# Performance work log

Measured on AMD Instinct MI355X. Metric: run time of the kernel, lower is better.

Reference implementation:

```python
import jax, jax.numpy as jnp
import numpy as np

B, C, H, W, K = 8, 128, 128, 128, 7


def _ln2d(x, gamma=None, beta=None, eps=1e-5):
    # LayerNorm2d: normalize over the channel dim at each (b, h, w) position
    mu = x.mean(axis=1, keepdims=True)
    var = x.var(axis=1, keepdims=True)
    y = (x - mu) * jax.lax.rsqrt(var + eps)
    if gamma is not None:
        y = y * gamma[None, :, None, None] + beta[None, :, None, None]
    return y


def _conv1x1(x, w, b):
    # w: [C_out, C_in] (1x1 conv collapsed)
    return jnp.einsum('oi,bihw->bohw', w, x) + b[None, :, None, None]


def _sym_conv(x, w):
    # channel-symmetric 7x7 conv, padding 'same' (SymmetricConv2d, symmetry_type='channel')
    ws = 0.5 * (w + jnp.swapaxes(w, 0, 1))
    return jax.lax.conv_general_dilated(
        x, ws, window_strides=(1, 1), padding='SAME',
        dimension_numbers=('NCHW', 'OIHW', 'NCHW'))


def setup_inputs() -> dict:
    key = jax.random.key(0)
    ks = jax.random.split(key, 8)
    f32 = jnp.float32
    return {
        'ff_input': jax.random.normal(ks[0], (B, C, H, W), f32),
        'h_exc': jax.random.normal(ks[1], (B, C, H, W), f32),
        'h_inh': jax.random.normal(ks[2], (B, C, H, W), f32),
        # 1x1 gate convs over concat([h_exc, h_inh, ff]) -> C channels
        'W_gain': jax.random.normal(ks[3], (C, 3 * C), f32) * 0.02,
        'b_gain': jnp.zeros((C,), f32),
        'W_mix': jax.random.normal(ks[4], (C, 3 * C), f32) * 0.02,
        'b_mix': jnp.zeros((C,), f32),
        # symmetric 7x7 horizontal connections
        'W_inh': jax.random.normal(ks[5], (C, C, K, K), f32) * 0.01,
        'W_exc': jax.random.normal(ks[6], (C, C, K, K), f32) * 0.01,
        # static circuit parameters (use_dynamic_parameters=False)
        'alpha': jnp.zeros((C,), f32),
        'mu': jnp.zeros((C,), f32),
        'kappa': jnp.ones((C,), f32) * 0.1,
        'omega': jnp.ones((C,), f32) * 0.1,
        # affine LayerNorm2d for circuit outputs c1/c2
        'c1_gamma': jnp.ones((C,), f32), 'c1_beta': jnp.zeros((C,), f32),
        'c2_gamma': jnp.ones((C,), f32), 'c2_beta': jnp.zeros((C,), f32),
    }


def reference(ff_input, h_exc, h_inh, W_gain, b_gain, W_mix, b_mix,
              W_inh, W_exc, alpha, mu, kappa, omega,
              c1_gamma, c1_beta, c2_gamma, c2_beta):
    # --- stage 1: gain gate (pre-norm on concat, 1x1 conv, sigmoid) ---
    g1_in = _ln2d(jnp.concatenate([h_exc, h_inh, ff_input], axis=1))  # [B,3C,H,W]
    g1 = jax.nn.sigmoid(_conv1x1(g1_in, W_gain, b_gain))              # [B,C,H,W]

    # --- stage 2: horizontal inhibition from gain-controlled excitatory state ---
    c1 = _ln2d(_sym_conv(h_exc * g1, W_inh), c1_gamma, c1_beta)

    # --- stage 3: input integration: divisive (alpha) + subtractive (mu) inhibition ---
    a = jax.nn.sigmoid(alpha)[None, :, None, None]  # force_alpha_divisive
    m = mu[None, :, None, None]
    inhibited = jax.nn.relu(ff_input - jax.nn.relu((a * h_inh + m) * c1))

    # --- stage 4: mix gate ---
    g2_in = _ln2d(jnp.concatenate([inhibited, h_exc, h_inh], axis=1))
    g2 = jax.nn.sigmoid(_conv1x1(g2_in, W_mix, b_mix))

    # --- stage 5: excitatory horizontal connections ---
    c2 = _ln2d(_sym_conv(inhibited, W_exc), c2_gamma, c2_beta)

    # --- stage 6: output integration (multiplicative excitation) ---
    k = kappa[None, :, None, None]
    o = jax.nn.relu(omega)[None, :, None, None]  # force_omega_nonnegative
    h_tilde = jax.nn.relu(k * (inhibited + c2) + o * (inhibited * c2))

    # --- gated state update of the excitatory population ---
    h_exc_new = (1.0 - g2) * h_exc + g2 * h_tilde
    return h_exc_new
```

## Files before the change

kernel.cpp:

```cpp
#include <hip/hip_runtime.h>
#include <cstddef>
#include <cstdint>

namespace {
constexpr int B_ = 8, C_ = 128, H_ = 128, W_ = 128;
constexpr int HW_ = H_ * W_;
constexpr size_t CHW_ = (size_t)C_ * HW_;
constexpr int NPIX_ = B_ * HW_;
}

typedef __attribute__((ext_vector_type(8))) short bf16x8;
typedef __attribute__((ext_vector_type(4))) float f32x4;
typedef __attribute__((ext_vector_type(2))) float f32x2;
typedef __attribute__((ext_vector_type(8))) unsigned short u16x8;
typedef __attribute__((ext_vector_type(4))) unsigned short u16x4;

__device__ inline unsigned short f2bf(float f) {
  unsigned int u = __float_as_uint(f);
  unsigned int r = u + 0x7FFFu + ((u >> 16) & 1u);
  return (unsigned short)(r >> 16);
}
__device__ inline float bf2f(unsigned short u) {
  return __uint_as_float((unsigned int)u << 16);
}

__device__ inline void async_copy16(void* lds_dst, const void* gsrc) {
  __builtin_amdgcn_global_load_lds(
      (const __attribute__((address_space(1))) unsigned int*)gsrc,
      (__attribute__((address_space(3))) unsigned int*)lds_dst, 16, 0, 0);
}

__global__ __launch_bounds__(256) void prep_w_bf16_k(
    const float* __restrict__ Wa, const float* __restrict__ Wb,
    unsigned short* __restrict__ Ta, unsigned short* __restrict__ Tb) {
  int idx = blockIdx.x * 256 + threadIdx.x;
  int j = idx & 7;
  int o = (idx >> 3) & 127;
  int g = (idx >> 10) & 15;
  int t = idx >> 14;
  int i = g * 8 + j;
  int ky = t / 7, kx = t - ky * 7;
  size_t oi = ((size_t)(o * 128 + i) * 7 + ky) * 7 + kx;
  size_t io = ((size_t)(i * 128 + o) * 7 + ky) * 7 + kx;
  Ta[idx] = f2bf(0.5f * (Wa[oi] + Wa[io]));
  Tb[idx] = f2bf(0.5f * (Wb[oi] + Wb[io]));
}

__global__ __launch_bounds__(256) void prep_apack_k(
    const float* __restrict__ Wg, const float* __restrict__ Wm,
    unsigned short* __restrict__ Ag, unsigned short* __restrict__ Am) {
  int idx = blockIdx.x * 256 + threadIdx.x;
  int j = idx & 7;
  int l = (idx >> 3) & 63;
  int f = (idx >> 9) & 7;
  int s = idx >> 12;
  int m = f * 16 + (l & 15);
  int k = s * 32 + (l >> 4) * 8 + j;
  Ag[idx] = f2bf(Wg[m * 384 + k]);
  Am[idx] = f2bf(Wm[m * 384 + k]);
}

__global__ void rowsum_k(const float* __restrict__ Wg,
                         const float* __restrict__ Wm,
                         const float* __restrict__ alpha,
                         float* __restrict__ rs, float* __restrict__ sa) {
  int t = threadIdx.x;
  const float* src = (t < 128) ? Wg : Wm;
  int row = t & 127;
  float s = 0.f;
  for (int i = 0; i < 384; ++i) s += bf2f(f2bf(src[row * 384 + i]));
  rs[t] = s;
  if (t < 128) sa[t] = 1.f / (1.f + __expf(-alpha[t]));
}

__global__ __launch_bounds__(256) void stats3_cvt_k(
    const float* __restrict__ t0, const float* __restrict__ t1,
    const float* __restrict__ t2, float* __restrict__ mu_o,
    float* __restrict__ inv_o, float* __restrict__ ps12,
    float* __restrict__ pq12, unsigned short* __restrict__ o0,
    unsigned short* __restrict__ o1, unsigned short* __restrict__ o2) {
  __shared__ unsigned short tile[64 * 136];
  __shared__ float s8[8][64];
  __shared__ float q8[8][64];
  int blk = blockIdx.x;
  int b = blk >> 8;
  int p0 = (blk & 255) * 64;
  int t = threadIdx.x;
  int px2 = (t & 31) * 2, cq = t >> 5;
  size_t base = (size_t)b * CHW_ + p0 + px2;
  int pixg = b * HW_ + p0;
  float s0a = 0.f, s0b = 0.f, q0a = 0.f, q0b = 0.f;
  for (int ci = 0; ci < 16; ++ci) {
    int c = cq * 16 + ci;
    f32x2 v = *(const f32x2*)(t0 + base + (size_t)c * HW_);
    s0a += v[0]; q0a = fmaf(v[0], v[0], q0a);
    s0b += v[1]; q0b = fmaf(v[1], v[1], q0b);
    tile[px2 * 136 + c] = f2bf(v[0]);
    tile[(px2 + 1) * 136 + c] = f2bf(v[1]);
  }
  __syncthreads();
#pragma unroll
  for (int pass = 0; pass < 4; ++pass) {
    int u = pass * 256 + t;
    int ppx = u >> 4, cg = u & 15;
    *(u16x8*)(o0 + (size_t)(pixg + ppx) * 128 + cg * 8) =
        *(const u16x8*)(tile + ppx * 136 + cg * 8);
  }
  __syncthreads();
  for (int ci = 0; ci < 16; ++ci) {
    int c = cq * 16 + ci;
    f32x2 v = *(const f32x2*)(t1 + base + (size_t)c * HW_);
    s0a += v[0]; q0a = fmaf(v[0], v[0], q0a);
    s0b += v[1]; q0b = fmaf(v[1], v[1], q0b);
    tile[px2 * 136 + c] = f2bf(v[0]);
    tile[(px2 + 1) * 136 + c] = f2bf(v[1]);
  }
  s8[cq][px2] = s0a;
  s8[cq][px2 + 1] = s0b;
  q8[cq][px2] = q0a;
  q8[cq][px2 + 1] = q0b;
  __syncthreads();
#pragma unroll
  for (int pass = 0; pass < 4; ++pass) {
    int u = pass * 256 + t;
    int ppx = u >> 4, cg = u & 15;
    *(u16x8*)(o1 + (size_t)(pixg + ppx) * 128 + cg * 8) =
        *(const u16x8*)(tile + ppx * 136 + cg * 8);
  }
  if (t < 64) {
    float ss = 0.f, qs = 0.f;
#pragma unroll
    for (int k = 0; k < 8; ++k) { ss += s8[k][t]; qs += q8[k][t]; }
    ps12[pixg + t] = ss;
    pq12[pixg + t] = qs;
  }
  __syncthreads();
  for (int ci = 0; ci < 16; ++ci) {
    int c = cq * 16 + ci;
    f32x2 v = *(const f32x2*)(t2 + base + (size_t)c * HW_);
    s0a += v[0]; q0a = fmaf(v[0], v[0], q0a);
    s0b += v[1]; q0b = fmaf(v[1], v[1], q0b);
    tile[px2 * 136 + c] = f2bf(v[0]);
    tile[(px2 + 1) * 136 + c] = f2bf(v[1]);
  }
  s8[cq][px2] = s0a;
  s8[cq][px2 + 1] = s0b;
  q8[cq][px2] = q0a;
  q8[cq][px2 + 1] = q0b;
  __syncthreads();
#pragma unroll
  for (int pass = 0; pass < 4; ++pass) {
    int u = pass * 256 + t;
    int ppx = u >> 4, cg = u & 15;
    *(u16x8*)(o2 + (size_t)(pixg + ppx) * 128 + cg * 8) =
        *(const u16x8*)(tile + ppx * 136 + cg * 8);
  }
  if (t < 64) {
    float ss = 0.f, qs = 0.f;
#pragma unroll
    for (int k = 0; k < 8; ++k) { ss += s8[k][t]; qs += q8[k][t]; }
    float m = ss * (1.f / 384.f);
    float var = qs * (1.f / 384.f) - m * m;
    mu_o[pixg + t] = m;
    inv_o[pixg + t] = rsqrtf(var + 1e-5f);
  }
}

template <int FINAL>
__global__ __launch_bounds__(256) void gemm_mfma_k(
    const unsigned short* __restrict__ Apack, const float* __restrict__ rowsum,
    const float* __restrict__ bias, const unsigned short* __restrict__ B0,
    const unsigned short* __restrict__ B1, const unsigned short* __restrict__ B2,
    const float* __restrict__ mu, const float* __restrict__ inv,
    const unsigned short* __restrict__ mult_cl, unsigned short* __restrict__ out_cl,
    const unsigned short* __restrict__ c2_cl, const float* __restrict__ muc,
    const float* __restrict__ invc, const unsigned short* __restrict__ inh_cl,
    const unsigned short* __restrict__ hexc_cl, const float* __restrict__ c2g,
    const float* __restrict__ c2b, const float* __restrict__ kap,
    const float* __restrict__ omg, float* __restrict__ out_f32) {
  int b = blockIdx.y;
  int tid = threadIdx.x;
  int lane = tid & 63, wid = tid >> 6;
  int l15 = lane & 15, kg = lane >> 4;
  int n0 = blockIdx.x * 128 + wid * 32;
  int pix0 = b * HW_ + n0;
  size_t bofs = (size_t)b * CHW_;
  f32x4 acc[8][2] = {};
#pragma unroll
  for (int s = 0; s < 12; ++s) {
    const unsigned short* src = (s < 4) ? B0 : ((s < 8) ? B1 : B2);
    int ch0 = (s & 3) * 32 + kg * 8;
    bf16x8 bfr[2];
#pragma unroll
    for (int nf = 0; nf < 2; ++nf)
      bfr[nf] = *(const bf16x8*)(src + (size_t)(pix0 + nf * 16 + l15) * 128 + ch0);
    const bf16x8* ap = (const bf16x8*)(Apack + ((size_t)(s * 8) * 64 + lane) * 8);
#pragma unroll
    for (int f = 0; f < 8; ++f) {
      bf16x8 afr = ap[f * 64];
#pragma unroll
      for (int nf = 0; nf < 2; ++nf)
        acc[f][nf] = __builtin_amdgcn_mfma_f32_16x16x32_bf16(afr, bfr[nf],
                                                             acc[f][nf], 0, 0, 0);
    }
  }
#pragma unroll
  for (int nf = 0; nf < 2; ++nf) {
    int n = n0 + nf * 16 + l15;
    int qpix = b * HW_ + n;
    float muv = mu[qpix], invv = inv[qpix];
    if (!FINAL) {
#pragma unroll
      for (int mf = 0; mf < 8; ++mf) {
        int m0 = mf * 16 + kg * 4;
        f32x4 rs4 = *(const f32x4*)(rowsum + m0);
        f32x4 bi4 = *(const f32x4*)(bias + m0);
        u16x4 mv = *(const u16x4*)(mult_cl + (size_t)qpix * 128 + m0);
        u16x4 st;
#pragma unroll
        for (int j = 0; j < 4; ++j) {
          float val = invv * (acc[mf][nf][j] - muv * rs4[j]) + bi4[j];
          float g = 1.f / (1.f + __expf(-val));
          st[j] = f2bf(bf2f(mv[j]) * g);
        }
        *(u16x4*)(out_cl + (size_t)qpix * 128 + m0) = st;
      }
    } else {
      float mcv = muc[qpix], icv = invc[qpix];
#pragma unroll
      for (int mf = 0; mf < 8; ++mf) {
        int m0 = mf * 16 + kg * 4;
        f32x4 rs4 = *(const f32x4*)(rowsum + m0);
        f32x4 bi4 = *(const f32x4*)(bias + m0);
        f32x4 g4 = *(const f32x4*)(c2g + m0);
        f32x4 b4 = *(const f32x4*)(c2b + m0);
        f32x4 k4 = *(const f32x4*)(kap + m0);
        f32x4 o4 = *(const f32x4*)(omg + m0);
        u16x4 c2v = *(const u16x4*)(c2_cl + (size_t)qpix * 128 + m0);
        u16x4 iv4 = *(const u16x4*)(inh_cl + (size_t)qpix * 128 + m0);
        u16x4 hx4 = *(const u16x4*)(hexc_cl + (size_t)qpix * 128 + m0);
#pragma unroll
        for (int j = 0; j < 4; ++j) {
          float val = invv * (acc[mf][nf][j] - muv * rs4[j]) + bi4[j];
          float g2 = 1.f / (1.f + __expf(-val));
          float c2 = (bf2f(c2v[j]) - mcv) * icv * g4[j] + b4[j];
          float iv = bf2f(iv4[j]);
          float ht =
              fmaxf(k4[j] * (iv + c2) + fmaxf(o4[j], 0.f) * (iv * c2), 0.f);
          out_f32[bofs + (size_t)(m0 + j) * HW_ + n] =
              (1.f - g2) * bf2f(hx4[j]) + g2 * ht;
        }
      }
    }
  }
}

__global__ __launch_bounds__(256, 2) void conv7_plain_k(
    const unsigned short* __restrict__ in_cl,
    const unsigned short* __restrict__ Wp, unsigned short* __restrict__ out,
    float* __restrict__ mu_o, float* __restrict__ inv_o) {
  __shared__ short w_s[7 * 4 * 128 * 8];
  __shared__ short in_s[2 * 4 * 136 * 8];
  int b = blockIdx.x & 7;
  int y0 = ((blockIdx.x >> 3) & 63) * 2;
  int tid = threadIdx.x;
  int lane = tid & 63;
  int wid = tid >> 6;
  int wm = wid >> 1;
  int row = wid & 1;
  int l15 = lane & 15, kg = lane >> 4;
  f32x4 acc[4][8] = {};
  for (int ky = 0; ky < 7; ++ky) {
    int ybase = y0 + ky - 3;
    for (int c4 = 0; c4 < 4; ++c4) {
      __syncthreads();
      const unsigned short* wsrc =
          Wp + (size_t)(ky * 7) * 16384 + c4 * 4096 + tid * 8;
#pragma unroll
      for (int kx = 0; kx < 7; ++kx) {
#pragma unroll
        for (int h = 0; h < 2; ++h) {
          async_copy16(w_s + kx * 4096 + (h * 256 + tid) * 8,
                       wsrc + kx * 16384 + h * 2048);
        }
      }
      for (int u = tid; u < 1088; u += 256) {
        int r = u / 544;
        int rem = u - r * 544;
        int g = rem / 136;
        int xi = rem - g * 136;
        int x = xi - 3;
        int y = ybase + r;
        u16x8 v = {};
        if (x >= 0 && x < 128 && y >= 0 && y < 128)
          v = *(const u16x8*)(in_cl + ((size_t)((b * 128 + y) * 128 + x) * 128 +
                                       c4 * 32 + g * 8));
        *(u16x8*)(in_s + u * 8) = v;
      }
      __syncthreads();
      for (int kx = 0; kx < 7; ++kx) {
        bf16x8 bfr[8], afr[4];
#pragma unroll
        for (int nf = 0; nf < 8; ++nf) {
          int xi = nf * 16 + l15 + kx;
          bfr[nf] = *(const bf16x8*)(in_s + ((row * 4 + kg) * 136 + xi) * 8);
        }
#pragma unroll
        for (int mf = 0; mf < 4; ++mf) {
          int oc = wm * 64 + mf * 16 + l15;
          afr[mf] = *(const bf16x8*)(w_s + ((kx * 4 + kg) * 128 + oc) * 8);
        }
#pragma unroll
        for (int mf = 0; mf < 4; ++mf)
#pragma unroll
          for (int nf = 0; nf < 8; ++nf)
            acc[mf][nf] = __builtin_amdgcn_mfma_f32_16x16x32_bf16(
                afr[mf], bfr[nf], acc[mf][nf], 0, 0, 0);
      }
    }
  }
  __syncthreads();
  float* red = (float*)in_s;
  int y = y0 + row;
#pragma unroll
  for (int nf = 0; nf < 8; ++nf) {
    int x = nf * 16 + l15;
    size_t paddr = (size_t)(b * HW_ + y * 128 + x) * 128;
    float s = 0.f, qq = 0.f;
#pragma unroll
    for (int mf = 0; mf < 4; ++mf) {
      int oc0 = wm * 64 + mf * 16 + kg * 4;
      u16x4 st;
#pragma unroll
      for (int j = 0; j < 4; ++j) {
        unsigned short bv = f2bf(acc[mf][nf][j]);
        float vr = bf2f(bv);
        s += vr;
        qq = fmaf(vr, vr, qq);
        st[j] = bv;
      }
      *(u16x4*)(out + paddr + oc0) = st;
    }
    s += __shfl_xor(s, 16);
    qq += __shfl_xor(qq, 16);
    s += __shfl_xor(s, 32);
    qq += __shfl_xor(qq, 32);
    if (kg == 0) {
      red[(wm * 2 + row) * 128 + x] = s;
      red[512 + (wm * 2 + row) * 128 + x] = qq;
    }
  }
  __syncthreads();
  {
    int r2 = tid >> 7, x2 = tid & 127;
    float s = red[r2 * 128 + x2] + red[(2 + r2) * 128 + x2];
    float qq = red[512 + r2 * 128 + x2] + red[512 + (2 + r2) * 128 + x2];
    float m = s * (1.f / 128.f);
    float var = qq * (1.f / 128.f) - m * m;
    int q = b * HW_ + (y0 + r2) * 128 + x2;
    mu_o[q] = m;
    inv_o[q] = rsqrtf(var + 1e-5f);
  }
}

__global__ __launch_bounds__(256, 2) void conv7_inh_k(
    const unsigned short* __restrict__ in_cl,
    const unsigned short* __restrict__ Wp, unsigned short* out,
    float* __restrict__ mu_o, float* __restrict__ inv_o,
    const unsigned short* ff_cl, const unsigned short* __restrict__ hinh_cl,
    const float* __restrict__ ps12, const float* __restrict__ pq12,
    const float* __restrict__ sig_alpha, const float* __restrict__ mu_p,
    const float* __restrict__ gamma, const float* __restrict__ beta) {
  __shared__ short w_s[7 * 4 * 128 * 8];
  __shared__ short in_s[2 * 4 * 136 * 8];
  int b = blockIdx.x & 7;
  int y0 = ((blockIdx.x >> 3) & 63) * 2;
  int tid = threadIdx.x;
  int lane = tid & 63;
  int wid = tid >> 6;
  int wm = wid >> 1;
  int row = wid & 1;
  int l15 = lane & 15, kg = lane >> 4;
  f32x4 acc[4][8] = {};
  for (int ky = 0; ky < 7; ++ky) {
    int ybase = y0 + ky - 3;
    for (int c4 = 0; c4 < 4; ++c4) {
      __syncthreads();
      const unsigned short* wsrc =
          Wp + (size_t)(ky * 7) * 16384 + c4 * 4096 + tid * 8;
#pragma unroll
      for (int kx = 0; kx < 7; ++kx) {
#pragma unroll
        for (int h = 0; h < 2; ++h) {
          async_copy16(w_s + kx * 4096 + (h * 256 + tid) * 8,
                       wsrc + kx * 16384 + h * 2048);
        }
      }
      for (int u = tid; u < 1088; u += 256) {
        int r = u / 544;
        int rem = u - r * 544;
        int g = rem / 136;
        int xi = rem - g * 136;
        int x = xi - 3;
        int y = ybase + r;
        u16x8 v = {};
        if (x >= 0 && x < 128 && y >= 0 && y < 128)
          v = *(const u16x8*)(in_cl + ((size_t)((b * 128 + y) * 128 + x) * 128 +
                                       c4 * 32 + g * 8));
        *(u16x8*)(in_s + u * 8) = v;
      }
      __syncthreads();
      for (int kx = 0; kx < 7; ++kx) {
        bf16x8 bfr[8], afr[4];
#pragma unroll
        for (int nf = 0; nf < 8; ++nf) {
          int xi = nf * 16 + l15 + kx;
          bfr[nf] = *(const bf16x8*)(in_s + ((row * 4 + kg) * 136 + xi) * 8);
        }
#pragma unroll
        for (int mf = 0; mf < 4; ++mf) {
          int oc = wm * 64 + mf * 16 + l15;
          afr[mf] = *(const bf16x8*)(w_s + ((kx * 4 + kg) * 128 + oc) * 8);
        }
#pragma unroll
        for (int mf = 0; mf < 4; ++mf)
#pragma unroll
          for (int nf = 0; nf < 8; ++nf)
            acc[mf][nf] = __builtin_amdgcn_mfma_f32_16x16x32_bf16(
                afr[mf], bfr[nf], acc[mf][nf], 0, 0, 0);
      }
    }
  }
  __syncthreads();
  float* red = (float*)in_s;
  int y = y0 + row;
#pragma unroll
  for (int nf = 0; nf < 8; ++nf) {
    int x = nf * 16 + l15;
    float s = 0.f, qq = 0.f;
#pragma unroll
    for (int mf = 0; mf < 4; ++mf) {
#pragma unroll
      for (int j = 0; j < 4; ++j) {
        float vr = bf2f(f2bf(acc[mf][nf][j]));
        s += vr;
        qq = fmaf(vr, vr, qq);
      }
    }
    s += __shfl_xor(s, 16);
    qq += __shfl_xor(qq, 16);
    s += __shfl_xor(s, 32);
    qq += __shfl_xor(qq, 32);
    if (kg == 0) {
      red[(wm * 2 + row) * 128 + x] = s;
      red[512 + (wm * 2 + row) * 128 + x] = qq;
    }
  }
  __syncthreads();
  {
    int r2 = tid >> 7, x2 = tid & 127;
    float s = red[r2 * 128 + x2] + red[(2 + r2) * 128 + x2];
    float qq = red[512 + r2 * 128 + x2] + red[512 + (2 + r2) * 128 + x2];
    float m = s * (1.f / 128.f);
    float var = qq * (1.f / 128.f) - m * m;
    red[1024 + r2 * 128 + x2] = m;
    red[1280 + r2 * 128 + x2] = rsqrtf(var + 1e-5f);
  }
  __syncthreads();
  f32x4 ga4[4], be4[4], sa4[4], mp4[4];
#pragma unroll
  for (int mf = 0; mf < 4; ++mf) {
    int oc0 = wm * 64 + mf * 16 + kg * 4;
    ga4[mf] = *(const f32x4*)(gamma + oc0);
    be4[mf] = *(const f32x4*)(beta + oc0);
    sa4[mf] = *(const f32x4*)(sig_alpha + oc0);
    mp4[mf] = *(const f32x4*)(mu_p + oc0);
  }
#pragma unroll
  for (int nf = 0; nf < 8; ++nf) {
    int x = nf * 16 + l15;
    float muv = red[1024 + row * 128 + x];
    float invv = red[1280 + row * 128 + x];
    size_t paddr = (size_t)(b * HW_ + y * 128 + x) * 128;
    float s2 = 0.f, q2 = 0.f;
#pragma unroll
    for (int mf = 0; mf < 4; ++mf) {
      int oc0 = wm * 64 + mf * 16 + kg * 4;
      u16x4 ffv = *(const u16x4*)(ff_cl + paddr + oc0);
      u16x4 hiv = *(const u16x4*)(hinh_cl + paddr + oc0);
      u16x4 st;
#pragma unroll
      for (int j = 0; j < 4; ++j) {
        float c1 =
            (bf2f(f2bf(acc[mf][nf][j])) - muv) * invv * ga4[mf][j] + be4[mf][j];
        float r = fmaxf((sa4[mf][j] * bf2f(hiv[j]) + mp4[mf][j]) * c1, 0.f);
        float v = fmaxf(bf2f(ffv[j]) - r, 0.f);
        unsigned short bv = f2bf(v);
        float vr = bf2f(bv);
        s2 += vr;
        q2 = fmaf(vr, vr, q2);
        st[j] = bv;
      }
      *(u16x4*)(out + paddr + oc0) = st;
    }
    s2 += __shfl_xor(s2, 16);
    q2 += __shfl_xor(q2, 16);
    s2 += __shfl_xor(s2, 32);
    q2 += __shfl_xor(q2, 32);
    if (kg == 0) {
      red[(wm * 2 + row) * 128 + x] = s2;
      red[512 + (wm * 2 + row) * 128 + x] = q2;
    }
  }
  __syncthreads();
  {
    int r2 = tid >> 7, x2 = tid & 127;
    float s = red[r2 * 128 + x2] + red[(2 + r2) * 128 + x2];
    float qq = red[512 + r2 * 128 + x2] + red[512 + (2 + r2) * 128 + x2];
    int pg = b * HW_ + (y0 + r2) * 128 + x2;
    s += ps12[pg];
    qq += pq12[pg];
    float m = s * (1.f / 384.f);
    float var = qq * (1.f / 384.f) - m * m;
    mu_o[pg] = m;
    inv_o[pg] = rsqrtf(var + 1e-5f);
  }
}

extern "C" void kernel_launch(void* const* d_in, const int* in_sizes, int n_in,
                              void* d_out, int out_size, void* d_ws,
                              size_t ws_size, hipStream_t stream) {
  const float* ff     = (const float*)d_in[0];
  const float* h_exc  = (const float*)d_in[1];
  const float* h_inh  = (const float*)d_in[2];
  const float* W_gain = (const float*)d_in[3];
  const float* b_gain = (const float*)d_in[4];
  const float* W_mix  = (const float*)d_in[5];
  const float* b_mix  = (const float*)d_in[6];
  const float* W_inh  = (const float*)d_in[7];
  const float* W_exc  = (const float*)d_in[8];
  const float* alpha  = (const float*)d_in[9];
  const float* mu_p   = (const float*)d_in[10];
  const float* kappa  = (const float*)d_in[11];
  const float* omega  = (const float*)d_in[12];
  const float* c1_g   = (const float*)d_in[13];
  const float* c1_b   = (const float*)d_in[14];
  const float* c2_g   = (const float*)d_in[15];
  const float* c2_b   = (const float*)d_in[16];

  float* w = (float*)d_ws;
  unsigned short* Wp_inh = (unsigned short*)w;  w += 401408;
  unsigned short* Wp_exc = (unsigned short*)w;  w += 401408;
  unsigned short* Ag     = (unsigned short*)w;  w += 24576;
  unsigned short* Am     = (unsigned short*)w;  w += 24576;
  float* rs     = w;  w += 256;
  float* sa     = w;  w += 128;
  float* mu1    = w;  w += NPIX_;
  float* inv1   = w;  w += NPIX_;
  float* mu2    = w;  w += NPIX_;
  float* inv2   = w;  w += NPIX_;
  float* mu_c2  = w;  w += NPIX_;
  float* inv_c2 = w;  w += NPIX_;
  float* ps12   = w;  w += NPIX_;
  float* pq12   = w;  w += NPIX_;
  unsigned short* exc_cl   = (unsigned short*)w;  w += 8388608;
  unsigned short* hinh_cl  = (unsigned short*)w;  w += 8388608;
  unsigned short* ffinh_cl = (unsigned short*)w;  w += 8388608;
  unsigned short* conv_cl  = (unsigned short*)w;  w += 8388608;

  unsigned short* gated_cl = (unsigned short*)d_out;

  prep_w_bf16_k<<<3136, 256, 0, stream>>>(W_inh, W_exc, Wp_inh, Wp_exc);
  prep_apack_k<<<192, 256, 0, stream>>>(W_gain, W_mix, Ag, Am);
  rowsum_k<<<1, 256, 0, stream>>>(W_gain, W_mix, alpha, rs, sa);

  stats3_cvt_k<<<2048, 256, 0, stream>>>(h_exc, h_inh, ff, mu1, inv1, ps12,
                                         pq12, exc_cl, hinh_cl, ffinh_cl);
  {
    dim3 g(128, 8);
    gemm_mfma_k<0><<<g, 256, 0, stream>>>(
        Ag, rs, b_gain, exc_cl, hinh_cl, ffinh_cl, mu1, inv1, exc_cl, gated_cl,
        nullptr, nullptr, nullptr, nullptr, nullptr, nullptr, nullptr, nullptr,
        nullptr, nullptr);
  }
  conv7_inh_k<<<512, 256, 0, stream>>>(gated_cl, Wp_inh, ffinh_cl, mu2, inv2,
                                       ffinh_cl, hinh_cl, ps12, pq12, sa, mu_p,
                                       c1_g, c1_b);
  conv7_plain_k<<<512, 256, 0, stream>>>(ffinh_cl, Wp_exc, conv_cl, mu_c2,
                                         inv_c2);
  {
    dim3 g(128, 8);
    gemm_mfma_k<1><<<g, 256, 0, stream>>>(
        Am, rs + 128, b_mix, ffinh_cl, exc_cl, hinh_cl, mu2, inv2, nullptr,
        nullptr, conv_cl, mu_c2, inv_c2, ffinh_cl, exc_cl, c2_g, c2_b, kappa,
        omega, (float*)d_out);
  }
}
```

Before: 591.3 us.

## Fuse gain-gate GEMM into stats/convert kernel using LDS-resident bf16 tiles

The first 1x1 gate GEMM is computed inside the stats/transpose kernel. MFMA operands are read directly from the shared-memory bf16 tile of each input as it is converted, and the LayerNorm stats are kept in shared memory. This removes a separate kernel launch that re-read the three channel-last tensors plus the mu/inv buffers from global memory. The cost is an extra 16KB shared buffer for h_exc, plus more registers and work per block, which could lower occupancy of the conversion kernel.

```diff
diff --git a/kernel.cpp b/kernel.cpp
--- a/kernel.cpp
+++ b/kernel.cpp
@@ -73,30 +73,41 @@
   if (t < 128) sa[t] = 1.f / (1.f + __expf(-alpha[t]));
 }
 
-__global__ __launch_bounds__(256) void stats3_cvt_k(
+__global__ __launch_bounds__(256) void stats3_gate_k(
     const float* __restrict__ t0, const float* __restrict__ t1,
-    const float* __restrict__ t2, float* __restrict__ mu_o,
-    float* __restrict__ inv_o, float* __restrict__ ps12,
-    float* __restrict__ pq12, unsigned short* __restrict__ o0,
-    unsigned short* __restrict__ o1, unsigned short* __restrict__ o2) {
+    const float* __restrict__ t2, const unsigned short* __restrict__ Apack,
+    const float* __restrict__ rowsum, const float* __restrict__ bias,
+    float* __restrict__ ps12, float* __restrict__ pq12,
+    unsigned short* __restrict__ o0, unsigned short* __restrict__ o1,
+    unsigned short* __restrict__ o2, unsigned short* __restrict__ gated_cl) {
   __shared__ unsigned short tile[64 * 136];
+  __shared__ unsigned short exc2[64 * 128];
   __shared__ float s8[8][64];
   __shared__ float q8[8][64];
+  __shared__ float bc_mu[64];
+  __shared__ float bc_inv[64];
   int blk = blockIdx.x;
   int b = blk >> 8;
   int p0 = (blk & 255) * 64;
   int t = threadIdx.x;
   int px2 = (t & 31) * 2, cq = t >> 5;
+  int lane = t & 63, wv = t >> 6;
+  int l15 = lane & 15, kg = lane >> 4;
   size_t base = (size_t)b * CHW_ + p0 + px2;
   int pixg = b * HW_ + p0;
+  f32x4 acc[8] = {};
   float s0a = 0.f, s0b = 0.f, q0a = 0.f, q0b = 0.f;
+
   for (int ci = 0; ci < 16; ++ci) {
     int c = cq * 16 + ci;
     f32x2 v = *(const f32x2*)(t0 + base + (size_t)c * HW_);
     s0a += v[0]; q0a = fmaf(v[0], v[0], q0a);
     s0b += v[1]; q0b = fmaf(v[1], v[1], q0b);
-    tile[px2 * 136 + c] = f2bf(v[0]);
-    tile[(px2 + 1) * 136 + c] = f2bf(v[1]);
+    unsigned short b0 = f2bf(v[0]), b1 = f2bf(v[1]);
+    tile[px2 * 136 + c] = b0;
+    tile[(px2 + 1) * 136 + c] = b1;
+    exc2[px2 * 128 + c] = b0;
+    exc2[(px2 + 1) * 128 + c] = b1;
   }
   __syncthreads();
 #pragma unroll
@@ -106,7 +117,19 @@
     *(u16x8*)(o0 + (size_t)(pixg + ppx) * 128 + cg * 8) =
         *(const u16x8*)(tile + ppx * 136 + cg * 8);
   }
-  __syncthreads();
+#pragma unroll
+  for (int sl = 0; sl < 4; ++sl) {
+    bf16x8 bfr =
+        *(const bf16x8*)(tile + (wv * 16 + l15) * 136 + sl * 32 + kg * 8);
+    const bf16x8* ap =
+        (const bf16x8*)(Apack + ((size_t)(sl * 8) * 64 + lane) * 8);
+#pragma unroll
+    for (int f = 0; f < 8; ++f)
+      acc[f] = __builtin_amdgcn_mfma_f32_16x16x32_bf16(ap[f * 64], bfr, acc[f],
+                                                       0, 0, 0);
+  }
+  __syncthreads();
+
   for (int ci = 0; ci < 16; ++ci) {
     int c = cq * 16 + ci;
     f32x2 v = *(const f32x2*)(t1 + base + (size_t)c * HW_);
@@ -127,6 +150,17 @@
     *(u16x8*)(o1 + (size_t)(pixg + ppx) * 128 + cg * 8) =
         *(const u16x8*)(tile + ppx * 136 + cg * 8);
   }
+#pragma unroll
+  for (int sl = 0; sl < 4; ++sl) {
+    bf16x8 bfr =
+        *(const bf16x8*)(tile + (wv * 16 + l15) * 136 + sl * 32 + kg * 8);
+    const bf16x8* ap =
+        (const bf16x8*)(Apack + ((size_t)((4 + sl) * 8) * 64 + lane) * 8);
+#pragma unroll
+    for (int f = 0; f < 8; ++f)
+      acc[f] = __builtin_amdgcn_mfma_f32_16x16x32_bf16(ap[f * 64], bfr, acc[f],
+                                                       0, 0, 0);
+  }
   if (t < 64) {
     float ss = 0.f, qs = 0.f;
 #pragma unroll
@@ -135,6 +169,7 @@
     pq12[pixg + t] = qs;
   }
   __syncthreads();
+
   for (int ci = 0; ci < 16; ++ci) {
     int c = cq * 16 + ci;
     f32x2 v = *(const f32x2*)(t2 + base + (size_t)c * HW_);
@@ -155,24 +190,55 @@
     *(u16x8*)(o2 + (size_t)(pixg + ppx) * 128 + cg * 8) =
         *(const u16x8*)(tile + ppx * 136 + cg * 8);
   }
+#pragma unroll
+  for (int sl = 0; sl < 4; ++sl) {
+    bf16x8 bfr =
+        *(const bf16x8*)(tile + (wv * 16 + l15) * 136 + sl * 32 + kg * 8);
+    const bf16x8* ap =
+        (const bf16x8*)(Apack + ((size_t)((8 + sl) * 8) * 64 + lane) * 8);
+#pragma unroll
+    for (int f = 0; f < 8; ++f)
+      acc[f] = __builtin_amdgcn_mfma_f32_16x16x32_bf16(ap[f * 64], bfr, acc[f],
+                                                       0, 0, 0);
+  }
   if (t < 64) {
     float ss = 0.f, qs = 0.f;
 #pragma unroll
     for (int k = 0; k < 8; ++k) { ss += s8[k][t]; qs += q8[k][t]; }
     float m = ss * (1.f / 384.f);
     float var = qs * (1.f / 384.f) - m * m;
-    mu_o[pixg + t] = m;
-    inv_o[pixg + t] = rsqrtf(var + 1e-5f);
-  }
-}
-
-template <int FINAL>
-__global__ __launch_bounds__(256) void gemm_mfma_k(
+    bc_mu[t] = m;
+    bc_inv[t] = rsqrtf(var + 1e-5f);
+  }
+  __syncthreads();
+
+  {
+    int pxl = wv * 16 + l15;
+    int pix = pixg + pxl;
+    float muv = bc_mu[pxl], invv = bc_inv[pxl];
+#pragma unroll
+    for (int f = 0; f < 8; ++f) {
+      int m0 = f * 16 + kg * 4;
+      f32x4 rs4 = *(const f32x4*)(rowsum + m0);
+      f32x4 bi4 = *(const f32x4*)(bias + m0);
+      u16x4 mv = *(const u16x4*)(exc2 + pxl * 128 + m0);
+      u16x4 st;
+#pragma unroll
+      for (int j = 0; j < 4; ++j) {
+        float val = invv * (acc[f][j] - muv * rs4[j]) + bi4[j];
+        float g = 1.f / (1.f + __expf(-val));
+        st[j] = f2bf(bf2f(mv[j]) * g);
+      }
+      *(u16x4*)(gated_cl + (size_t)pix * 128 + m0) = st;
+    }
+  }
+}
+
+__global__ __launch_bounds__(256) void gemm_final_k(
     const unsigned short* __restrict__ Apack, const float* __restrict__ rowsum,
     const float* __restrict__ bias, const unsigned short* __restrict__ B0,
     const unsigned short* __restrict__ B1, const unsigned short* __restrict__ B2,
     const float* __restrict__ mu, const float* __restrict__ inv,
-    const unsigned short* __restrict__ mult_cl, unsigned short* __restrict__ out_cl,
     const unsigned short* __restrict__ c2_cl, const float* __restrict__ muc,
     const float* __restrict__ invc, const unsigned short* __restrict__ inh_cl,
     const unsigned short* __restrict__ hexc_cl, const float* __restrict__ c2g,
@@ -209,47 +275,29 @@
     int n = n0 + nf * 16 + l15;
     int qpix = b * HW_ + n;
     float muv = mu[qpix], invv = inv[qpix];
-    if (!FINAL) {
-#pragma unroll
-      for (int mf = 0; mf < 8; ++mf) {
-        int m0 = mf * 16 + kg * 4;
-        f32x4 rs4 = *(const f32x4*)(rowsum + m0);
-        f32x4 bi4 = *(const f32x4*)(bias + m0);
-        u16x4 mv = *(const u16x4*)(mult_cl + (size_t)qpix * 128 + m0);
-        u16x4 st;
-#pragma unroll
-        for (int j = 0; j < 4; ++j) {
-          float val = invv * (acc[mf][nf][j] - muv * rs4[j]) + bi4[j];
-          float g = 1.f / (1.f + __expf(-val));
-          st[j] = f2bf(bf2f(mv[j]) * g);
-        }
-        *(u16x4*)(out_cl + (size_t)qpix * 128 + m0) = st;
-      }
-    } else {
-      float mcv = muc[qpix], icv = invc[qpix];
-#pragma unroll
-      for (int mf = 0; mf < 8; ++mf) {
-        int m0 = mf * 16 + kg * 4;
-        f32x4 rs4 = *(const f32x4*)(rowsum + m0);
-        f32x4 bi4 = *(const f32x4*)(bias + m0);
-        f32x4 g4 = *(const f32x4*)(c2g + m0);
-        f32x4 b4 = *(const f32x4*)(c2b + m0);
-        f32x4 k4 = *(const f32x4*)(kap + m0);
-        f32x4 o4 = *(const f32x4*)(omg + m0);
-        u16x4 c2v = *(const u16x4*)(c2_cl + (size_t)qpix * 128 + m0);
-        u16x4 iv4 = *(const u16x4*)(inh_cl + (size_t)qpix * 128 + m0);
-        u16x4 hx4 = *(const u16x4*)(hexc_cl + (size_t)qpix * 128 + m0);
-#pragma unroll
-        for (int j = 0; j < 4; ++j) {
-          float val = invv * (acc[mf][nf][j] - muv * rs4[j]) + bi4[j];
-          float g2 = 1.f / (1.f + __expf(-val));
-          float c2 = (bf2f(c2v[j]) - mcv) * icv * g4[j] + b4[j];
-          float iv = bf2f(iv4[j]);
-          float ht =
-              fmaxf(k4[j] * (iv + c2) + fmaxf(o4[j], 0.f) * (iv * c2), 0.f);
-          out_f32[bofs + (size_t)(m0 + j) * HW_ + n] =
-              (1.f - g2) * bf2f(hx4[j]) + g2 * ht;
-        }
+    float mcv = muc[qpix], icv = invc[qpix];
+#pragma unroll
+    for (int mf = 0; mf < 8; ++mf) {
+      int m0 = mf * 16 + kg * 4;
+      f32x4 rs4 = *(const f32x4*)(rowsum + m0);
+      f32x4 bi4 = *(const f32x4*)(bias + m0);
+      f32x4 g4 = *(const f32x4*)(c2g + m0);
+      f32x4 b4 = *(const f32x4*)(c2b + m0);
+      f32x4 k4 = *(const f32x4*)(kap + m0);
+      f32x4 o4 = *(const f32x4*)(omg + m0);
+      u16x4 c2v = *(const u16x4*)(c2_cl + (size_t)qpix * 128 + m0);
+      u16x4 iv4 = *(const u16x4*)(inh_cl + (size_t)qpix * 128 + m0);
+      u16x4 hx4 = *(const u16x4*)(hexc_cl + (size_t)qpix * 128 + m0);
+#pragma unroll
+      for (int j = 0; j < 4; ++j) {
+        float val = invv * (acc[mf][nf][j] - muv * rs4[j]) + bi4[j];
+        float g2 = 1.f / (1.f + __expf(-val));
+        float c2 = (bf2f(c2v[j]) - mcv) * icv * g4[j] + b4[j];
+        float iv = bf2f(iv4[j]);
+        float ht =
+            fmaxf(k4[j] * (iv + c2) + fmaxf(o4[j], 0.f) * (iv * c2), 0.f);
+        out_f32[bofs + (size_t)(m0 + j) * HW_ + n] =
+            (1.f - g2) * bf2f(hx4[j]) + g2 * ht;
       }
     }
   }
@@ -555,8 +603,6 @@
   unsigned short* Am     = (unsigned short*)w;  w += 24576;
   float* rs     = w;  w += 256;
   float* sa     = w;  w += 128;
-  float* mu1    = w;  w += NPIX_;
-  float* inv1   = w;  w += NPIX_;
   float* mu2    = w;  w += NPIX_;
   float* inv2   = w;  w += NPIX_;
   float* mu_c2  = w;  w += NPIX_;
@@ -574,15 +620,9 @@
   prep_apack_k<<<192, 256, 0, stream>>>(W_gain, W_mix, Ag, Am);
   rowsum_k<<<1, 256, 0, stream>>>(W_gain, W_mix, alpha, rs, sa);
 
-  stats3_cvt_k<<<2048, 256, 0, stream>>>(h_exc, h_inh, ff, mu1, inv1, ps12,
-                                         pq12, exc_cl, hinh_cl, ffinh_cl);
-  {
-    dim3 g(128, 8);
-    gemm_mfma_k<0><<<g, 256, 0, stream>>>(
-        Ag, rs, b_gain, exc_cl, hinh_cl, ffinh_cl, mu1, inv1, exc_cl, gated_cl,
-        nullptr, nullptr, nullptr, nullptr, nullptr, nullptr, nullptr, nullptr,
-        nullptr, nullptr);
-  }
+  stats3_gate_k<<<2048, 256, 0, stream>>>(h_exc, h_inh, ff, Ag, rs, b_gain,
+                                          ps12, pq12, exc_cl, hinh_cl,
+                                          ffinh_cl, gated_cl);
   conv7_inh_k<<<512, 256, 0, stream>>>(gated_cl, Wp_inh, ffinh_cl, mu2, inv2,
                                        ffinh_cl, hinh_cl, ps12, pq12, sa, mu_p,
                                        c1_g, c1_b);
@@ -590,9 +630,9 @@
                                          inv_c2);
   {
     dim3 g(128, 8);
-    gemm_mfma_k<1><<<g, 256, 0, stream>>>(
-        Am, rs + 128, b_mix, ffinh_cl, exc_cl, hinh_cl, mu2, inv2, nullptr,
-        nullptr, conv_cl, mu_c2, inv_c2, ffinh_cl, exc_cl, c2_g, c2_b, kappa,
-        omega, (float*)d_out);
-  }
-}
+    gemm_final_k<<<g, 256, 0, stream>>>(
+        Am, rs + 128, b_mix, ffinh_cl, exc_cl, hinh_cl, mu2, inv2, conv_cl,
+        mu_c2, inv_c2, ffinh_cl, exc_cl, c2_g, c2_b, kappa, omega,
+        (float*)d_out);
+  }
+}
```

New measurement: 561.9 us. 1.05x faster.
